# Optimization experiments

Measured on AMD Instinct MI355X. Metric: run time of the kernel, lower is better.

The kernel has to match this reference:

```python
import jax, jax.numpy as jnp
import numpy as np

N_HEADS = 16
ATT_DIM = 1024
HEAD_DIM = ATT_DIM // N_HEADS
SCALE = 1.0 / (HEAD_DIM ** 0.5)


def setup_inputs() -> dict:
    key = jax.random.key(0)
    k1, k2 = jax.random.split(key)
    B, N, D = 4, 2048, 1024
    X = jax.random.normal(k1, (B, N, D), dtype=jnp.float32)
    W_qkv = jax.random.normal(k2, (3 * ATT_DIM, D), dtype=jnp.float32) * 0.02  # trunc_normal-ish std
    return {"X": X, "W_qkv": W_qkv}


def reference(X, W_qkv):
    B, N, D = X.shape
    # qkv projection (bias=False): X @ W^T -> [b, n, 3*att_dim]
    QKV = jnp.einsum('bnd,od->bno', X, W_qkv)
    # rearrange 'b n (p h d) -> p b h n d'
    QKV = QKV.reshape(B, N, 3, N_HEADS, HEAD_DIM).transpose(2, 0, 3, 1, 4)
    Q, K, V = QKV[0], QKV[1], QKV[2]
    # scaled dot-product attention, full NxN scores (as in source)
    scores = jnp.einsum('bhid,bhjd->bhij', Q, K) * SCALE
    S = jax.nn.softmax(scores, axis=-1)
    # dropout rate is 0.0 -> identity
    Y = jnp.einsum('bhij,bhjd->bhid', S, V)
    # 'b h n d -> b n (h d)'; out_proj is Identity (out_dim == att_dim)
    return Y.transpose(0, 2, 1, 3).reshape(B, N, N_HEADS * HEAD_DIM)
```

## Files before the change

kernel.cpp:

```cpp
#include <hip/hip_runtime.h>

#define BATCH   4
#define SEQ     2048
#define DMODEL  1024
#define NHEADS  16
#define HDIM    64
#define QSC     0.18033688f

typedef short s16x8 __attribute__((ext_vector_type(8)));
typedef float f32x4 __attribute__((ext_vector_type(4)));
typedef const __attribute__((address_space(1))) unsigned int* gas_t;
typedef __attribute__((address_space(3))) unsigned int* las_t;

__device__ inline unsigned short f2bf(float f) {
    unsigned int u = __float_as_uint(f);
    u += 0x7FFF + ((u >> 16) & 1);
    return (unsigned short)(u >> 16);
}

__device__ __forceinline__ float exp2_fast(float x) {
#if __has_builtin(__builtin_amdgcn_exp2f)
    return __builtin_amdgcn_exp2f(x);
#else
    return exp2f(x);
#endif
}

__device__ __forceinline__ float rcp_fast(float x) {
#if __has_builtin(__builtin_amdgcn_rcpf)
    return __builtin_amdgcn_rcpf(x);
#else
    return 1.0f / x;
#endif
}

__device__ __forceinline__ unsigned int pack_bf16x2(float lo, float hi) {
    unsigned int a = __float_as_uint(lo) + 0x8000u;
    unsigned int b = __float_as_uint(hi) + 0x8000u;
#if __has_builtin(__builtin_amdgcn_perm)
    return __builtin_amdgcn_perm(b, a, 0x07060302u);
#else
    return (a >> 16) | (b & 0xFFFF0000u);
#endif
}

__global__ void cvt_bf16_2(const float* __restrict__ a,
                           unsigned short* __restrict__ oa, int n4a,
                           const float* __restrict__ bsrc,
                           unsigned short* __restrict__ ob, int n4b) {
    int i = blockIdx.x * blockDim.x + threadIdx.x;
    if (i < n4a) {
        float4 v = ((const float4*)a)[i];
        ushort4 o;
        o.x = f2bf(v.x); o.y = f2bf(v.y); o.z = f2bf(v.z); o.w = f2bf(v.w);
        ((ushort4*)oa)[i] = o;
    } else {
        int j = i - n4a;
        if (j < n4b) {
            float4 v = ((const float4*)bsrc)[j];
            ushort4 o;
            o.x = f2bf(v.x); o.y = f2bf(v.y); o.z = f2bf(v.z); o.w = f2bf(v.w);
            ((ushort4*)ob)[j] = o;
        }
    }
}

__global__ __launch_bounds__(256) void qkv_gemm(
    const unsigned short* __restrict__ Xb,
    const unsigned short* __restrict__ Wb,
    unsigned short* __restrict__ Qo,
    unsigned short* __restrict__ Ko,
    unsigned short* __restrict__ Vt)
{
    __shared__ __align__(16) unsigned short As[2 * 128 * 32];
    __shared__ __align__(16) unsigned short Bs[2 * 128 * 32];

    const int t    = threadIdx.x;
    const int flat = blockIdx.y * 24 + blockIdx.x;
    const int sw   = (flat & 7) * 192 + (flat >> 3);
    const int m0   = (sw / 24) * 128;
    const int n0   = (sw % 24) * 128;

    const int wid  = t >> 6;
    const int lane = t & 63;
    const int l15  = lane & 15;
    const int quad = lane >> 4;
    const int wm   = (wid >> 1) * 64;
    const int wn   = (wid & 1) * 64;

    const int rA   = wid * 32 + (lane >> 2);
    const int kcol_phys = (lane & 3) * 8;
    const int kcol_src  = ((lane & 3) ^ ((rA >> 1) & 3)) * 8;
    const unsigned short* gA = &Xb[(size_t)(m0 + rA) * 1024 + kcol_src];
    const unsigned short* gB = &Wb[(size_t)(n0 + rA) * 1024 + kcol_src];

    const int cswq = (quad ^ ((l15 >> 1) & 3)) * 8;

    f32x4 acc[4][4] = {};

    auto stage = [&](int k0, int bufE) {
        #pragma unroll
        for (int rd = 0; rd < 2; rd++) {
            __builtin_amdgcn_global_load_lds(
                (gas_t)(const void*)(gA + rd * 16 * 1024 + k0),
                (las_t)(void*)&As[bufE + (rA + rd * 16) * 32 + kcol_phys], 16, 0, 0);
            __builtin_amdgcn_global_load_lds(
                (gas_t)(const void*)(gB + rd * 16 * 1024 + k0),
                (las_t)(void*)&Bs[bufE + (rA + rd * 16) * 32 + kcol_phys], 16, 0, 0);
        }
    };

    auto comp = [&](int bufE) {
        s16x8 af[4], bf[4];
        #pragma unroll
        for (int mt = 0; mt < 4; mt++)
            af[mt] = *(const s16x8*)&As[bufE + (wm + mt * 16 + l15) * 32 + cswq];
        #pragma unroll
        for (int nt = 0; nt < 4; nt++)
            bf[nt] = *(const s16x8*)&Bs[bufE + (wn + nt * 16 + l15) * 32 + cswq];
        #pragma unroll
        for (int mt = 0; mt < 4; mt++)
            #pragma unroll
            for (int nt = 0; nt < 4; nt++)
                acc[mt][nt] = __builtin_amdgcn_mfma_f32_16x16x32_bf16(
                    af[mt], bf[nt], acc[mt][nt], 0, 0, 0);
    };

    stage(0, 0);
    __syncthreads();

    #pragma unroll 1
    for (int k0 = 0; k0 < 1024; k0 += 64) {
        stage(k0 + 32, 4096);
        comp(0);
        __syncthreads();
        if (k0 + 64 < 1024) stage(k0 + 64, 0);
        comp(4096);
        __syncthreads();
    }

    #pragma unroll
    for (int mt = 0; mt < 4; mt++) {
        const int mbase = m0 + wm + mt * 16 + quad * 4;
        const int b     = mbase >> 11;
        const int nbase = mbase & 2047;
        #pragma unroll
        for (int nt = 0; nt < 4; nt++) {
            const int o  = n0 + wn + nt * 16 + l15;
            const int p  = o >> 10;
            const int oo = o & 1023;
            const int h  = oo >> 6;
            const int d  = oo & 63;
            if (p == 0) {
                #pragma unroll
                for (int r = 0; r < 4; r++)
                    Qo[((size_t)(b * 16 + h) * 2048 + nbase + r) * 64 + d] =
                        f2bf(acc[mt][nt][r] * QSC);
            } else if (p == 1) {
                #pragma unroll
                for (int r = 0; r < 4; r++)
                    Ko[((size_t)(b * 16 + h) * 2048 + nbase + r) * 64 + d] =
                        f2bf(acc[mt][nt][r]);
            } else {
                ushort4 v4;
                v4.x = f2bf(acc[mt][nt][0]);
                v4.y = f2bf(acc[mt][nt][1]);
                v4.z = f2bf(acc[mt][nt][2]);
                v4.w = f2bf(acc[mt][nt][3]);
                *(ushort4*)&Vt[((size_t)(b * 16 + h) * 64 + d) * 2048 + nbase] = v4;
            }
        }
    }
}

#define PSTRIDE 72
#define PBASE   16384

__global__ __launch_bounds__(256) void attn(
    const unsigned short* __restrict__ Q,
    const unsigned short* __restrict__ K,
    const unsigned short* __restrict__ Vt,
    float* __restrict__ out)
{
    __shared__ __align__(16) unsigned short LDS[PBASE + 4 * 32 * PSTRIDE];

    const int t    = threadIdx.x;
    const int w    = t >> 6;
    const int lane = t & 63;
    const int l15  = lane & 15;
    const int quad = lane >> 4;
    const int head = blockIdx.y;
    const int b    = head >> 4;
    const int h    = head & 15;
    const int q0   = blockIdx.x * 128 + w * 32;

    const unsigned short* Qh = Q  + (size_t)head * 2048 * 64;
    const unsigned short* Kh = K  + (size_t)head * 2048 * 64;
    const unsigned short* Vh = Vt + (size_t)head * 64 * 2048;

    const int r0 = t >> 3;
    const int c0 = (t & 7) ^ (r0 & 7);
    const unsigned short* srcK = Kh + r0 * 64 + c0 * 8;
    const unsigned short* srcV = Vh + r0 * 2048 + c0 * 8;

    auto stageKV = [&](int kt, int bufE) {
        #pragma unroll
        for (int rd = 0; rd < 2; rd++) {
            __builtin_amdgcn_global_load_lds(
                (gas_t)(const void*)(srcK + kt * 4096 + rd * 2048),
                (las_t)(void*)&LDS[bufE + rd * 2048 + w * 512], 16, 0, 0);
            __builtin_amdgcn_global_load_lds(
                (gas_t)(const void*)(srcV + kt * 64 + rd * 65536),
                (las_t)(void*)&LDS[bufE + 4096 + rd * 2048 + w * 512], 16, 0, 0);
        }
    };

    s16x8 qb[2][2];
    #pragma unroll
    for (int mt = 0; mt < 2; mt++)
        #pragma unroll
        for (int kc = 0; kc < 2; kc++)
            qb[mt][kc] = *(const s16x8*)&Qh[(size_t)(q0 + mt * 16 + l15) * 64 + kc * 32 + quad * 8];

    s16x8 onesf;
    #pragma unroll
    for (int i = 0; i < 8; i++) onesf[i] = (short)0x3F80;
    const f32x4 fz = {0.f, 0.f, 0.f, 0.f};

    f32x4 y[2][4] = {};
    f32x4 ysum[2] = {};
    unsigned short* P = &LDS[PBASE + w * (32 * PSTRIDE)];

    const int x7   = l15 & 7;
    const int csw0 = (quad ^ x7) * 8;
    const int csw1 = ((4 + quad) ^ x7) * 8;

    auto compute = [&](int bufE) {
        s16x8 kb[4][2];
        #pragma unroll
        for (int nt = 0; nt < 4; nt++) {
            const int rowb = bufE + (nt * 16 + l15) * 64;
            kb[nt][0] = *(const s16x8*)&LDS[rowb + csw0];
            kb[nt][1] = *(const s16x8*)&LDS[rowb + csw1];
        }
        __builtin_amdgcn_s_setprio(1);
        f32x4 st[4][2];
        #pragma unroll
        for (int nt = 0; nt < 4; nt++)
            #pragma unroll
            for (int mt = 0; mt < 2; mt++)
                st[nt][mt] = __builtin_amdgcn_mfma_f32_16x16x32_bf16(
                    kb[nt][0], qb[mt][0], fz, 0, 0, 0);
        #pragma unroll
        for (int nt = 0; nt < 4; nt++)
            #pragma unroll
            for (int mt = 0; mt < 2; mt++)
                st[nt][mt] = __builtin_amdgcn_mfma_f32_16x16x32_bf16(
                    kb[nt][1], qb[mt][1], st[nt][mt], 0, 0, 0);
        __builtin_amdgcn_s_setprio(0);
        s16x8 vb[4][2];
        #pragma unroll
        for (int dt = 0; dt < 4; dt++) {
            const int rowb = bufE + 4096 + (dt * 16 + l15) * 64;
            vb[dt][0] = *(const s16x8*)&LDS[rowb + csw0];
            vb[dt][1] = *(const s16x8*)&LDS[rowb + csw1];
        }
        #pragma unroll
        for (int mt = 0; mt < 2; mt++)
            #pragma unroll
            for (int nt = 0; nt < 4; nt++) {
                float p0 = exp2_fast(st[nt][mt][0]);
                float p1 = exp2_fast(st[nt][mt][1]);
                float p2 = exp2_fast(st[nt][mt][2]);
                float p3 = exp2_fast(st[nt][mt][3]);
                uint2 u;
                u.x = pack_bf16x2(p0, p1);
                u.y = pack_bf16x2(p2, p3);
                *(uint2*)&P[(mt * 16 + l15) * PSTRIDE + nt * 16 + quad * 4] = u;
            }
        __builtin_amdgcn_s_setprio(1);
        #pragma unroll
        for (int kc = 0; kc < 2; kc++) {
            s16x8 pa[2];
            #pragma unroll
            for (int mt = 0; mt < 2; mt++)
                pa[mt] = *(const s16x8*)&P[(mt * 16 + l15) * PSTRIDE + kc * 32 + quad * 8];
            #pragma unroll
            for (int mt = 0; mt < 2; mt++)
                ysum[mt] = __builtin_amdgcn_mfma_f32_16x16x32_bf16(
                    pa[mt], onesf, ysum[mt], 0, 0, 0);
            #pragma unroll
            for (int mt = 0; mt < 2; mt++)
                #pragma unroll
                for (int dt = 0; dt < 4; dt++)
                    y[mt][dt] = __builtin_amdgcn_mfma_f32_16x16x32_bf16(
                        pa[mt], vb[dt][kc], y[mt][dt], 0, 0, 0);
        }
        __builtin_amdgcn_s_setprio(0);
    };

    stageKV(0, 0);
    __syncthreads();

    #pragma unroll 1
    for (int kt = 0; kt < 32; kt += 2) {
        stageKV(kt + 1, 8192);
        compute(0);
        __syncthreads();
        if (kt + 2 < 32) stageKV(kt + 2, 0);
        compute(8192);
        __syncthreads();
    }

    float rinv[2][4];
    #pragma unroll
    for (int mt = 0; mt < 2; mt++)
        #pragma unroll
        for (int r = 0; r < 4; r++)
            rinv[mt][r] = rcp_fast(ysum[mt][r]);

    #pragma unroll
    for (int mt = 0; mt < 2; mt++)
        #pragma unroll
        for (int dt = 0; dt < 4; dt++)
            #pragma unroll
            for (int r = 0; r < 4; r++) {
                const int n = q0 + mt * 16 + quad * 4 + r;
                const int d = dt * 16 + l15;
                out[((size_t)(b * 2048 + n)) * 1024 + h * 64 + d] =
                    y[mt][dt][r] * rinv[mt][r];
            }
}

extern "C" void kernel_launch(void* const* d_in, const int* in_sizes, int n_in,
                              void* d_out, int out_size, void* d_ws, size_t ws_size,
                              hipStream_t stream) {
    const float* X = (const float*)d_in[0];
    const float* W = (const float*)d_in[1];
    float* out = (float*)d_out;

    char* ws = (char*)d_ws;
    unsigned short* Xb = (unsigned short*)(ws);
    unsigned short* Wb = (unsigned short*)(ws + 16777216);
    unsigned short* Qb = (unsigned short*)(ws + 23068672);
    unsigned short* Kb = (unsigned short*)(ws + 39845888);
    unsigned short* Vt = (unsigned short*)(ws + 56623104);

    cvt_bf16_2<<<dim3(11264), dim3(256), 0, stream>>>(X, Xb, 2097152, W, Wb, 786432);
    qkv_gemm<<<dim3(24, 64), dim3(256), 0, stream>>>(Xb, Wb, Qb, Kb, Vt);
    attn<<<dim3(16, 64), dim3(256), 0, stream>>>(Qb, Kb, Vt, out);
}
```

Before: 249.5 us.

## Load V fragments directly from global memory instead of staging in LDS

V tiles are no longer staged into shared memory; each wave reads its V MFMA operands straight from global memory per key tile, while only K goes through the double-buffered LDS path. This halves LDS use per block, which may allow more blocks per CU, and removes the LDS traffic for V. The cost is that every wave in a block re-reads the same V data from global/L2 with no prefetch ahead of use. The s_setprio hints around the MFMA sections are also removed.

```diff
diff --git a/kernel.cpp b/kernel.cpp
--- a/kernel.cpp
+++ b/kernel.cpp
@@ -174,7 +174,7 @@
 }
 
 #define PSTRIDE 72
-#define PBASE   16384
+#define PBASE   8192
 
 __global__ __launch_bounds__(256) void attn(
     const unsigned short* __restrict__ Q,
@@ -201,17 +201,13 @@
     const int r0 = t >> 3;
     const int c0 = (t & 7) ^ (r0 & 7);
     const unsigned short* srcK = Kh + r0 * 64 + c0 * 8;
-    const unsigned short* srcV = Vh + r0 * 2048 + c0 * 8;
-
-    auto stageKV = [&](int kt, int bufE) {
+
+    auto stageK = [&](int kt, int bufE) {
         #pragma unroll
         for (int rd = 0; rd < 2; rd++) {
             __builtin_amdgcn_global_load_lds(
                 (gas_t)(const void*)(srcK + kt * 4096 + rd * 2048),
                 (las_t)(void*)&LDS[bufE + rd * 2048 + w * 512], 16, 0, 0);
-            __builtin_amdgcn_global_load_lds(
-                (gas_t)(const void*)(srcV + kt * 64 + rd * 65536),
-                (las_t)(void*)&LDS[bufE + 4096 + rd * 2048 + w * 512], 16, 0, 0);
         }
     };
 
@@ -235,7 +231,15 @@
     const int csw0 = (quad ^ x7) * 8;
     const int csw1 = ((4 + quad) ^ x7) * 8;
 
-    auto compute = [&](int bufE) {
+    const unsigned short* vbase = Vh + (size_t)l15 * 2048 + quad * 8;
+
+    auto compute = [&](int kt, int bufE) {
+        s16x8 vb[4][2];
+        #pragma unroll
+        for (int dt = 0; dt < 4; dt++)
+            #pragma unroll
+            for (int kc = 0; kc < 2; kc++)
+                vb[dt][kc] = *(const s16x8*)&vbase[(size_t)dt * 16 * 2048 + kt * 64 + kc * 32];
         s16x8 kb[4][2];
         #pragma unroll
         for (int nt = 0; nt < 4; nt++) {
@@ -243,7 +247,6 @@
             kb[nt][0] = *(const s16x8*)&LDS[rowb + csw0];
             kb[nt][1] = *(const s16x8*)&LDS[rowb + csw1];
         }
-        __builtin_amdgcn_s_setprio(1);
         f32x4 st[4][2];
         #pragma unroll
         for (int nt = 0; nt < 4; nt++)
@@ -257,14 +260,6 @@
             for (int mt = 0; mt < 2; mt++)
                 st[nt][mt] = __builtin_amdgcn_mfma_f32_16x16x32_bf16(
                     kb[nt][1], qb[mt][1], st[nt][mt], 0, 0, 0);
-        __builtin_amdgcn_s_setprio(0);
-        s16x8 vb[4][2];
-        #pragma unroll
-        for (int dt = 0; dt < 4; dt++) {
-            const int rowb = bufE + 4096 + (dt * 16 + l15) * 64;
-            vb[dt][0] = *(const s16x8*)&LDS[rowb + csw0];
-            vb[dt][1] = *(const s16x8*)&LDS[rowb + csw1];
-        }
         #pragma unroll
         for (int mt = 0; mt < 2; mt++)
             #pragma unroll
@@ -278,7 +273,6 @@
                 u.y = pack_bf16x2(p2, p3);
                 *(uint2*)&P[(mt * 16 + l15) * PSTRIDE + nt * 16 + quad * 4] = u;
             }
-        __builtin_amdgcn_s_setprio(1);
         #pragma unroll
         for (int kc = 0; kc < 2; kc++) {
             s16x8 pa[2];
@@ -296,19 +290,18 @@
                     y[mt][dt] = __builtin_amdgcn_mfma_f32_16x16x32_bf16(
                         pa[mt], vb[dt][kc], y[mt][dt], 0, 0, 0);
         }
-        __builtin_amdgcn_s_setprio(0);
     };
 
-    stageKV(0, 0);
+    stageK(0, 0);
     __syncthreads();
 
     #pragma unroll 1
     for (int kt = 0; kt < 32; kt += 2) {
-        stageKV(kt + 1, 8192);
-        compute(0);
+        stageK(kt + 1, 4096);
+        compute(kt, 0);
         __syncthreads();
-        if (kt + 2 < 32) stageKV(kt + 2, 0);
-        compute(8192);
+        if (kt + 2 < 32) stageK(kt + 2, 0);
+        compute(kt + 1, 4096);
         __syncthreads();
     }
 
```

Result: slower. 297.3 us (+19.2%).

## Restructure QKV GEMM with K=64 tiles and finer-grained staged prefetch pipeline

Applied to the files above, without the earlier changes.

Rewrites the QKV projection GEMM to use 64-wide K tiles with an XOR swizzle, and lays the four waves out 1x4 along N so each wave covers all 128 rows and a 32-column slice. Each K step is split into four sub-phases. Each phase issues a quarter of the next tile's global-to-LDS loads, and explicit vmcnt waits plus raw s_barriers replace __syncthreads. The aim is to overlap memory traffic with MFMA work more finely and halve the loop trip count. Separately, it removes the s_setprio hints from the attention kernel, which may change how waves interleave there.

```diff
diff --git a/kernel.cpp b/kernel.cpp
--- a/kernel.cpp
+++ b/kernel.cpp
@@ -72,8 +72,8 @@
     unsigned short* __restrict__ Ko,
     unsigned short* __restrict__ Vt)
 {
-    __shared__ __align__(16) unsigned short As[2 * 128 * 32];
-    __shared__ __align__(16) unsigned short Bs[2 * 128 * 32];
+    __shared__ __align__(16) unsigned short As[2 * 8192];
+    __shared__ __align__(16) unsigned short Bs[2 * 8192];
 
     const int t    = threadIdx.x;
     const int flat = blockIdx.y * 24 + blockIdx.x;
@@ -81,72 +81,148 @@
     const int m0   = (sw / 24) * 128;
     const int n0   = (sw % 24) * 128;
 
-    const int wid  = t >> 6;
+    const int wn   = t >> 6;
     const int lane = t & 63;
     const int l15  = lane & 15;
     const int quad = lane >> 4;
-    const int wm   = (wid >> 1) * 64;
-    const int wn   = (wid & 1) * 64;
-
-    const int rA   = wid * 32 + (lane >> 2);
-    const int kcol_phys = (lane & 3) * 8;
-    const int kcol_src  = ((lane & 3) ^ ((rA >> 1) & 3)) * 8;
-    const unsigned short* gA = &Xb[(size_t)(m0 + rA) * 1024 + kcol_src];
-    const unsigned short* gB = &Wb[(size_t)(n0 + rA) * 1024 + kcol_src];
-
-    const int cswq = (quad ^ ((l15 >> 1) & 3)) * 8;
-
-    f32x4 acc[4][4] = {};
-
-    auto stage = [&](int k0, int bufE) {
-        #pragma unroll
-        for (int rd = 0; rd < 2; rd++) {
+
+    const int srow = t >> 3;
+    const int csrc = ((t & 7) ^ (srow & 7)) * 8;
+    const unsigned short* gA = &Xb[(size_t)(m0 + srow) * 1024 + csrc];
+    const unsigned short* gB = &Wb[(size_t)(n0 + srow) * 1024 + csrc];
+    const int ldst = t * 8;
+
+    const int x7  = l15 & 7;
+    const int ck0 = (quad ^ x7) * 8;
+    const int ck1 = ((4 + quad) ^ x7) * 8;
+
+    f32x4 acc[8][2] = {};
+
+    auto stageA = [&](int h, int kt, int bufE) {
+        #pragma unroll
+        for (int r = 0; r < 2; r++)
             __builtin_amdgcn_global_load_lds(
-                (gas_t)(const void*)(gA + rd * 16 * 1024 + k0),
-                (las_t)(void*)&As[bufE + (rA + rd * 16) * 32 + kcol_phys], 16, 0, 0);
+                (gas_t)(const void*)(gA + h * 65536 + r * 32768 + kt * 64),
+                (las_t)(void*)&As[bufE + h * 4096 + r * 2048 + ldst], 16, 0, 0);
+    };
+    auto stageB = [&](int h, int kt, int bufE) {
+        #pragma unroll
+        for (int r = 0; r < 2; r++)
             __builtin_amdgcn_global_load_lds(
-                (gas_t)(const void*)(gB + rd * 16 * 1024 + k0),
-                (las_t)(void*)&Bs[bufE + (rA + rd * 16) * 32 + kcol_phys], 16, 0, 0);
-        }
+                (gas_t)(const void*)(gB + h * 65536 + r * 32768 + kt * 64),
+                (las_t)(void*)&Bs[bufE + h * 4096 + r * 2048 + ldst], 16, 0, 0);
     };
 
-    auto comp = [&](int bufE) {
-        s16x8 af[4], bf[4];
-        #pragma unroll
-        for (int mt = 0; mt < 4; mt++)
-            af[mt] = *(const s16x8*)&As[bufE + (wm + mt * 16 + l15) * 32 + cswq];
-        #pragma unroll
-        for (int nt = 0; nt < 4; nt++)
-            bf[nt] = *(const s16x8*)&Bs[bufE + (wn + nt * 16 + l15) * 32 + cswq];
-        #pragma unroll
-        for (int mt = 0; mt < 4; mt++)
-            #pragma unroll
-            for (int nt = 0; nt < 4; nt++)
-                acc[mt][nt] = __builtin_amdgcn_mfma_f32_16x16x32_bf16(
-                    af[mt], bf[nt], acc[mt][nt], 0, 0, 0);
-    };
-
-    stage(0, 0);
-    __syncthreads();
+    stageB(0, 0, 0); stageB(1, 0, 0); stageA(0, 0, 0); stageA(1, 0, 0);
+    asm volatile("s_waitcnt vmcnt(2)" ::: "memory");
+    __builtin_amdgcn_s_barrier();
+    asm volatile("" ::: "memory");
 
     #pragma unroll 1
-    for (int k0 = 0; k0 < 1024; k0 += 64) {
-        stage(k0 + 32, 4096);
-        comp(0);
-        __syncthreads();
-        if (k0 + 64 < 1024) stage(k0 + 64, 0);
-        comp(4096);
-        __syncthreads();
+    for (int kt = 0; kt < 16; kt++) {
+        const int buf  = (kt & 1) * 8192;
+        const int obuf = 8192 - buf;
+        const int ktn  = (kt < 15) ? kt + 1 : 15;
+
+        {
+            s16x8 af[4], bf[2];
+            #pragma unroll
+            for (int i = 0; i < 4; i++)
+                af[i] = *(const s16x8*)&As[buf + (i * 16 + l15) * 64 + ck0];
+            #pragma unroll
+            for (int j = 0; j < 2; j++)
+                bf[j] = *(const s16x8*)&Bs[buf + (wn * 32 + j * 16 + l15) * 64 + ck0];
+            stageB(0, ktn, obuf);
+            asm volatile("" ::: "memory");
+            __builtin_amdgcn_s_barrier();
+            asm volatile("" ::: "memory");
+            #pragma unroll
+            for (int i = 0; i < 4; i++)
+                #pragma unroll
+                for (int j = 0; j < 2; j++)
+                    acc[i][j] = __builtin_amdgcn_mfma_f32_16x16x32_bf16(
+                        af[i], bf[j], acc[i][j], 0, 0, 0);
+            asm volatile("" ::: "memory");
+            __builtin_amdgcn_s_barrier();
+            asm volatile("" ::: "memory");
+        }
+        {
+            s16x8 af[4], bf[2];
+            #pragma unroll
+            for (int i = 0; i < 4; i++)
+                af[i] = *(const s16x8*)&As[buf + (i * 16 + l15) * 64 + ck1];
+            #pragma unroll
+            for (int j = 0; j < 2; j++)
+                bf[j] = *(const s16x8*)&Bs[buf + (wn * 32 + j * 16 + l15) * 64 + ck1];
+            stageB(1, ktn, obuf);
+            asm volatile("s_waitcnt vmcnt(4)" ::: "memory");
+            __builtin_amdgcn_s_barrier();
+            asm volatile("" ::: "memory");
+            #pragma unroll
+            for (int i = 0; i < 4; i++)
+                #pragma unroll
+                for (int j = 0; j < 2; j++)
+                    acc[i][j] = __builtin_amdgcn_mfma_f32_16x16x32_bf16(
+                        af[i], bf[j], acc[i][j], 0, 0, 0);
+            asm volatile("" ::: "memory");
+            __builtin_amdgcn_s_barrier();
+            asm volatile("" ::: "memory");
+        }
+        {
+            s16x8 af[4], bf[2];
+            #pragma unroll
+            for (int i = 0; i < 4; i++)
+                af[i] = *(const s16x8*)&As[buf + (64 + i * 16 + l15) * 64 + ck0];
+            #pragma unroll
+            for (int j = 0; j < 2; j++)
+                bf[j] = *(const s16x8*)&Bs[buf + (wn * 32 + j * 16 + l15) * 64 + ck0];
+            stageA(0, ktn, obuf);
+            asm volatile("" ::: "memory");
+            __builtin_amdgcn_s_barrier();
+            asm volatile("" ::: "memory");
+            #pragma unroll
+            for (int i = 0; i < 4; i++)
+                #pragma unroll
+                for (int j = 0; j < 2; j++)
+                    acc[4 + i][j] = __builtin_amdgcn_mfma_f32_16x16x32_bf16(
+                        af[i], bf[j], acc[4 + i][j], 0, 0, 0);
+            asm volatile("" ::: "memory");
+            __builtin_amdgcn_s_barrier();
+            asm volatile("" ::: "memory");
+        }
+        {
+            s16x8 af[4], bf[2];
+            #pragma unroll
+            for (int i = 0; i < 4; i++)
+                af[i] = *(const s16x8*)&As[buf + (64 + i * 16 + l15) * 64 + ck1];
+            #pragma unroll
+            for (int j = 0; j < 2; j++)
+                bf[j] = *(const s16x8*)&Bs[buf + (wn * 32 + j * 16 + l15) * 64 + ck1];
+            stageA(1, ktn, obuf);
+            asm volatile("s_waitcnt vmcnt(2)" ::: "memory");
+            __builtin_amdgcn_s_barrier();
+            asm volatile("" ::: "memory");
+            #pragma unroll
+            for (int i = 0; i < 4; i++)
+                #pragma unroll
+                for (int j = 0; j < 2; j++)
+                    acc[4 + i][j] = __builtin_amdgcn_mfma_f32_16x16x32_bf16(
+                        af[i], bf[j], acc[4 + i][j], 0, 0, 0);
+            asm volatile("" ::: "memory");
+            __builtin_amdgcn_s_barrier();
+            asm volatile("" ::: "memory");
+        }
     }
+    asm volatile("s_waitcnt vmcnt(0)" ::: "memory");
 
     #pragma unroll
-    for (int mt = 0; mt < 4; mt++) {
-        const int mbase = m0 + wm + mt * 16 + quad * 4;
+    for (int mrep = 0; mrep < 8; mrep++) {
+        const int mbase = m0 + mrep * 16 + quad * 4;
         const int b     = mbase >> 11;
         const int nbase = mbase & 2047;
         #pragma unroll
-        for (int nt = 0; nt < 4; nt++) {
-            const int o  = n0 + wn + nt * 16 + l15;
+        for (int nrep = 0; nrep < 2; nrep++) {
+            const int o  = n0 + wn * 32 + nrep * 16 + l15;
             const int p  = o >> 10;
             const int oo = o & 1023;
             const int h  = oo >> 6;
@@ -155,18 +231,18 @@
                 #pragma unroll
                 for (int r = 0; r < 4; r++)
                     Qo[((size_t)(b * 16 + h) * 2048 + nbase + r) * 64 + d] =
-                        f2bf(acc[mt][nt][r] * QSC);
+                        f2bf(acc[mrep][nrep][r] * QSC);
             } else if (p == 1) {
                 #pragma unroll
                 for (int r = 0; r < 4; r++)
                     Ko[((size_t)(b * 16 + h) * 2048 + nbase + r) * 64 + d] =
-                        f2bf(acc[mt][nt][r]);
+                        f2bf(acc[mrep][nrep][r]);
             } else {
                 ushort4 v4;
-                v4.x = f2bf(acc[mt][nt][0]);
-                v4.y = f2bf(acc[mt][nt][1]);
-                v4.z = f2bf(acc[mt][nt][2]);
-                v4.w = f2bf(acc[mt][nt][3]);
+                v4.x = f2bf(acc[mrep][nrep][0]);
+                v4.y = f2bf(acc[mrep][nrep][1]);
+                v4.z = f2bf(acc[mrep][nrep][2]);
+                v4.w = f2bf(acc[mrep][nrep][3]);
                 *(ushort4*)&Vt[((size_t)(b * 16 + h) * 64 + d) * 2048 + nbase] = v4;
             }
         }
@@ -243,7 +319,6 @@
             kb[nt][0] = *(const s16x8*)&LDS[rowb + csw0];
             kb[nt][1] = *(const s16x8*)&LDS[rowb + csw1];
         }
-        __builtin_amdgcn_s_setprio(1);
         f32x4 st[4][2];
         #pragma unroll
         for (int nt = 0; nt < 4; nt++)
@@ -257,7 +332,6 @@
             for (int mt = 0; mt < 2; mt++)
                 st[nt][mt] = __builtin_amdgcn_mfma_f32_16x16x32_bf16(
                     kb[nt][1], qb[mt][1], st[nt][mt], 0, 0, 0);
-        __builtin_amdgcn_s_setprio(0);
         s16x8 vb[4][2];
         #pragma unroll
         for (int dt = 0; dt < 4; dt++) {
@@ -278,7 +352,6 @@
                 u.y = pack_bf16x2(p2, p3);
                 *(uint2*)&P[(mt * 16 + l15) * PSTRIDE + nt * 16 + quad * 4] = u;
             }
-        __builtin_amdgcn_s_setprio(1);
         #pragma unroll
         for (int kc = 0; kc < 2; kc++) {
             s16x8 pa[2];
@@ -296,7 +369,6 @@
                     y[mt][dt] = __builtin_amdgcn_mfma_f32_16x16x32_bf16(
                         pa[mt], vb[dt][kc], y[mt][dt], 0, 0, 0);
         }
-        __builtin_amdgcn_s_setprio(0);
     };
 
     stageKV(0, 0);
```

Result: no change. 251.0 us (+0.6%).
